# Kernel tuning notes

Measured on AMD Instinct MI355X. Metric: run time of the kernel, lower is better.

Reference implementation:

```python
import jax, jax.numpy as jnp
import numpy as np

N, D, O, H, T, S, R, BN = 4096, 256, 256, 256, 512, 8, 4, 2  # nodes, in, out, hidden, text_len, adj_size, relations used, basis_num


def setup_inputs() -> dict:
    key = jax.random.key(0)
    ks = jax.random.split(key, 16)
    sc = 0.05
    return {
        "entity_embeddings": jax.random.normal(ks[0], (N, D), jnp.float32) * sc,
        "text_encodings": jax.random.normal(ks[1], (1, T, 2 * H), jnp.float32) * sc,
        "adj_to_use": jnp.arange(R, dtype=jnp.int32),
        "adj_masks": jax.random.randint(ks[2], (R, N, N), 0, 2, dtype=jnp.int32),
        "text_guids": jax.random.normal(ks[3], (S, 2 * H), jnp.float32) * sc,
        "graph_guids_1": jax.random.normal(ks[4], (S, D), jnp.float32) * sc,
        "graph_guids_2": jax.random.normal(ks[5], (S, D), jnp.float32) * sc,
        "guid_a": jax.random.normal(ks[6], (S,), jnp.float32),
        "basis_V": jax.random.normal(ks[7], (D, BN, O), jnp.float32) * sc,
        "basis_b": jax.random.normal(ks[8], (S, BN), jnp.float32) * sc,
        "W_1": jax.random.normal(ks[9], (2 * H, D), jnp.float32) * sc,
        "W_2": jax.random.normal(ks[10], (2 * H, D), jnp.float32) * sc,
        "ln_gamma": jnp.ones((O,), jnp.float32),
        "ln_beta": jnp.zeros((O,), jnp.float32),
    }


def reference(entity_embeddings, text_encodings, adj_to_use, adj_masks,
              text_guids, graph_guids_1, graph_guids_2, guid_a,
              basis_V, basis_b, W_1, W_2, ln_gamma, ln_beta):
    te = text_encodings[0]                                  # [T, 2H] (batch of 1)
    tg = text_guids[adj_to_use]                             # [R, 2H]
    # text attention: softmax over T, per relation
    att = jax.nn.softmax(te @ tg.T, axis=0)                 # [T, R]
    context = att.T @ te                                    # [R, 2H]
    c1 = context @ W_1                                      # [R, D]
    c2 = context @ W_2
    ga = jax.nn.sigmoid(guid_a[adj_to_use])[:, None]        # [R, 1]
    g1 = ga * graph_guids_1[adj_to_use] + (1.0 - ga) * c1   # [R, D]
    g2 = ga * graph_guids_2[adj_to_use] + (1.0 - ga) * c2
    s1 = entity_embeddings @ g1.T                           # [N, R]
    s2 = entity_embeddings @ g2.T
    # A[r,i,j] = s1[i,r] + s2[j,r], masked softmax over j
    A = s1.T[:, :, None] + s2.T[:, None, :]                 # [R, N, N]
    A = jnp.where(adj_masks == 1, A, jnp.float32(-1e10))
    A = jax.nn.softmax(A, axis=-1)
    fused = jnp.einsum('rij,jd->rid', A, entity_embeddings) # [R, N, D]
    # torch.cat over relations on last dim -> column index r*D + d
    fused_cat = jnp.transpose(fused, (1, 0, 2)).reshape(N, R * D)
    # torch.matmul([R,BN],[D,BN,O]) -> [D,R,O], then .view(R*D, O) (row index d*R + r)
    bb = basis_b[adj_to_use]                                # [R, BN]
    W = jnp.einsum('rb,dbo->dro', bb, basis_V).reshape(D * R, O)
    out = fused_cat @ W                                     # [N, O]
    mu = jnp.mean(out, axis=-1, keepdims=True)
    var = jnp.var(out, axis=-1, keepdims=True)
    out = (out - mu) / jnp.sqrt(var + 1e-5) * ln_gamma + ln_beta
    return jax.nn.relu(out)
```

## Files before the change

kernel.cpp:

```cpp
#include <hip/hip_runtime.h>
#include <hip/hip_bf16.h>


typedef unsigned short u16;
typedef short bf16x8 __attribute__((ext_vector_type(8)));
typedef float f32x4 __attribute__((ext_vector_type(4)));
typedef int   v4i   __attribute__((ext_vector_type(4)));
typedef unsigned int v2u __attribute__((ext_vector_type(2)));

#define G2_OFF    0
#define E2_OFF    4096
#define WRT_OFF   69632
#define FPT_OFF   593920
#define FUSED_OFF 9506816
#define CAN_OFF   26284032

#define C_ENT 0
#define C_TE  1048576
#define C_TG  1310720
#define C_GG2 1314816
#define C_GA  1316864
#define C_BV  1316872
#define C_BB  1447944
#define C_W2  1447960
#define C_GAM 1579032
#define C_BET 1579288

__device__ __forceinline__ float b2f(u16 u) {
    union { unsigned int i; float f; } v; v.i = ((unsigned int)u) << 16; return v.f;
}
__device__ __forceinline__ u16 f2b(float f) {
    union { float f; unsigned int i; } v; v.f = f;
    return (u16)((v.i + 0x7FFFu + ((v.i >> 16) & 1u)) >> 16);
}

__global__ __launch_bounds__(256) void k_cvt(
    const void* s0, const void* s1, const void* s2, const void* s3,
    const void* s4, const void* s5, const void* s6, const void* s7,
    const void* s8, const void* s9, const unsigned* __restrict__ graw,
    u16* __restrict__ dst)
{
    bool isbf = (graw[0] == 0x3F803F80u);
    const void* srcs[10] = {s0, s1, s2, s3, s4, s5, s6, s7, s8, s9};
    const int ns[10]     = {1048576, 262144, 4096, 2048, 8, 131072, 16, 131072, 256, 256};
    const int offs[10]   = {C_ENT, C_TE, C_TG, C_GG2, C_GA, C_BV, C_BB, C_W2, C_GAM, C_BET};
    const int bstart[11] = {0, 512, 640, 642, 643, 644, 708, 709, 773, 774, 775};
    int b = blockIdx.x, a = 0;
    while (b >= bstart[a + 1]) ++a;
    int rel = b - bstart[a];
    int n = ns[a];
    u16* d = dst + offs[a];
    int base = rel * 2048 + threadIdx.x;
    if (isbf) {
        const u16* s = (const u16*)srcs[a];
        for (int k = 0; k < 8; ++k) { int i = base + k * 256; if (i < n) d[i] = s[i]; }
    } else {
        const float* s = (const float*)srcs[a];
        for (int k = 0; k < 8; ++k) { int i = base + k * 256; if (i < n) d[i] = f2b(s[i]); }
    }
}

__global__ __launch_bounds__(1024) void k_pre(const u16* __restrict__ te,
                                              const int* __restrict__ adj,
                                              const u16* __restrict__ tguids,
                                              const u16* __restrict__ gg2,
                                              const u16* __restrict__ guida,
                                              const u16* __restrict__ W2,
                                              float* __restrict__ g2ws) {
    __shared__ float s_tg[4 * 512];
    __shared__ float s_att[512 * 4];
    __shared__ float s_red[512 * 4];
    __shared__ float s_ctx[4 * 512];
    int tid = threadIdx.x;
    int a[4] = {adj[0], adj[1], adj[2], adj[3]};
    for (int idx = tid; idx < 2048; idx += 1024) {
        int r = idx >> 9, h = idx & 511;
        s_tg[r * 512 + h] = b2f(tguids[a[r] * 512 + h]);
    }
    __syncthreads();
    if (tid < 512) {
        float s[4] = {0.f, 0.f, 0.f, 0.f};
        const u16* row = te + tid * 512;
        for (int h = 0; h < 512; ++h) {
            float tv = b2f(row[h]);
            s[0] += tv * s_tg[h]; s[1] += tv * s_tg[512 + h];
            s[2] += tv * s_tg[1024 + h]; s[3] += tv * s_tg[1536 + h];
        }
        for (int r = 0; r < 4; ++r) { s_att[tid * 4 + r] = s[r]; s_red[tid * 4 + r] = s[r]; }
    }
    __syncthreads();
    for (int st = 256; st > 0; st >>= 1) {
        if (tid < st) for (int r = 0; r < 4; ++r)
            s_red[tid * 4 + r] = fmaxf(s_red[tid * 4 + r], s_red[(tid + st) * 4 + r]);
        __syncthreads();
    }
    float mx[4]; for (int r = 0; r < 4; ++r) mx[r] = s_red[r];
    __syncthreads();
    if (tid < 512) for (int r = 0; r < 4; ++r) {
        float e = __expf(s_att[tid * 4 + r] - mx[r]);
        s_att[tid * 4 + r] = e; s_red[tid * 4 + r] = e;
    }
    __syncthreads();
    for (int st = 256; st > 0; st >>= 1) {
        if (tid < st) for (int r = 0; r < 4; ++r)
            s_red[tid * 4 + r] += s_red[(tid + st) * 4 + r];
        __syncthreads();
    }
    float dn[4]; for (int r = 0; r < 4; ++r) dn[r] = s_red[r];
    __syncthreads();
    if (tid < 512) for (int r = 0; r < 4; ++r) s_att[tid * 4 + r] /= dn[r];
    __syncthreads();
    for (int rep = 0; rep < 2; ++rep) {
        int o = tid + rep * 1024; int r = o >> 9, h = o & 511;
        float acc = 0.f;
        for (int t = 0; t < 512; ++t) acc += s_att[t * 4 + r] * b2f(te[t * 512 + h]);
        s_ctx[r * 512 + h] = acc;
    }
    __syncthreads();
    {
        int r = tid >> 8, d = tid & 255;
        float acc = 0.f;
        for (int h = 0; h < 512; ++h) acc += s_ctx[r * 512 + h] * b2f(W2[h * 256 + d]);
        float gav = 1.f / (1.f + expf(-b2f(guida[a[r]])));
        g2ws[r * 256 + d] = gav * b2f(gg2[a[r] * 256 + d]) + (1.f - gav) * acc;
    }
}

__global__ __launch_bounds__(256) void k_s2_wrt(const u16* __restrict__ entity,
                                                const int* __restrict__ adj,
                                                const u16* __restrict__ basisV,
                                                const u16* __restrict__ basisb,
                                                const float* __restrict__ g2ws,
                                                float* __restrict__ e2ws,
                                                u16* __restrict__ wrt) {
    int b = blockIdx.x, tid = threadIdx.x;
    if (b < 64) {
        int j = b * 64 + (tid >> 2), r = tid & 3;
        const u16* erow = entity + j * 256;
        const float* g2r = g2ws + r * 256;
        float acc = 0.f;
        for (int d = 0; d < 256; ++d) acc += b2f(erow[d]) * g2r[d];
        e2ws[r * 4096 + j] = expf(acc);
    } else {
        int b2 = b - 64; int r = b2 >> 6;
        int c = (b2 & 63) * 4 + (tid >> 6);
        int dq = tid & 63;
        int dbase = dq * 4;
        int a[4] = {adj[0], adj[1], adj[2], adj[3]};
        for (int dd = 0; dd < 4; ++dd) {
            float w = 0.f;
            for (int bi = 0; bi < 2; ++bi)
                w += b2f(basisb[a[dd] * 2 + bi]) * b2f(basisV[((64 * r + dq) * 2 + bi) * 256 + c]);
            wrt[(r * 256 + c) * 256 + dbase + dd] = f2b(w);
        }
    }
}

__global__ __launch_bounds__(256) void k_fplus(const u16* __restrict__ entity,
                                               const u16* __restrict__ wrt,
                                               const float* __restrict__ e2ws,
                                               u16* __restrict__ fpt) {
    int b = blockIdx.x, tid = threadIdx.x;
    if (b < 256) {
        int r = b & 3, ct = (b >> 2) & 3, jt = b >> 4;
        int c0 = ct * 64, j0 = jt * 256;
        __shared__ __align__(16) u16 lw[64 * 264];
        const u16* wr = wrt + (r * 256 + c0) * 256;
        for (int k = 0; k < 8; ++k) {
            int ci = tid + k * 256; int row = ci >> 5, off = (ci & 31) * 8;
            *(v4i*)(&lw[row * 264 + off]) = *(const v4i*)(wr + row * 256 + off);
        }
        __syncthreads();
        int wave = tid >> 6, ln = tid & 15, q = (tid & 63) >> 4;
        f32x4 acc[4][4] = {};
        for (int ks = 0; ks < 8; ++ks) {
            bf16x8 afr[4], bfr[4];
            for (int mt = 0; mt < 4; ++mt)
                afr[mt] = *(const bf16x8*)(&lw[(mt * 16 + ln) * 264 + ks * 32 + q * 8]);
            for (int nt = 0; nt < 4; ++nt) {
                int j = j0 + (wave * 4 + nt) * 16 + ln;
                bfr[nt] = *(const bf16x8*)(entity + j * 256 + ks * 32 + q * 8);
            }
            for (int mt = 0; mt < 4; ++mt)
                for (int nt = 0; nt < 4; ++nt)
                    acc[mt][nt] = __builtin_amdgcn_mfma_f32_16x16x32_bf16(afr[mt], bfr[nt], acc[mt][nt], 0, 0, 0);
        }
        for (int nt = 0; nt < 4; ++nt) {
            int j = j0 + (wave * 4 + nt) * 16 + ln;
            float e2j = e2ws[r * 4096 + j];
            int kt = j >> 5, kk = j & 31;
            u16* dst = fpt + (((size_t)(r * 128 + kt)) * 272 << 5);
            for (int mt = 0; mt < 4; ++mt)
                for (int reg = 0; reg < 4; ++reg) {
                    int c = c0 + mt * 16 + q * 4 + reg;
                    dst[(c << 5) + kk] = f2b(acc[mt][nt][reg] * e2j);
                }
        }
    } else {
        int b2 = b - 256; int r = b2 >> 1, half = b2 & 1;
        const float* e2r = e2ws + r * 4096;
        for (int it = 0; it < 128; ++it) {
            int l = it * 256 + tid;
            int kk = l & 31;
            int c  = 256 + ((l >> 5) & 15);
            int kt = half * 64 + (l >> 9);
            fpt[(((size_t)(r * 128 + kt) * 272 + c) << 5) + kk] =
                (c == 256) ? f2b(e2r[kt * 32 + kk]) : (u16)0;
        }
    }
}

__global__ __launch_bounds__(512) void k_big(const int* __restrict__ masks,
                                             const u16* __restrict__ fpt,
                                             float* __restrict__ fused) {
    __shared__ __align__(16) u16 lm[64 * 40];
    __shared__ __align__(16) u16 lf[272 * 40];
    __shared__ float lden[64];
    int b = blockIdx.x, tid = threadIdx.x;
    int xcd = b & 7; int r = xcd & 3;
    int it = (b >> 3) + ((xcd >> 2) << 5);
    long i0 = (long)it * 64;
    const int* mbase = masks + ((long)r << 24) + i0 * 4096;
    const u16* fbase = fpt + (size_t)r * 128 * 272 * 32;
    int mrow = tid >> 3, mch = tid & 7;
    int wave = tid >> 6, lane = tid & 63, ln = lane & 15, q = lane >> 4;
    int mg = wave >> 2, ng = wave & 3;

    f32x4 acc[2][4] = {};
    f32x4 accD0 = {}, accD1 = {};

    v4i pmA, pf0A, pf1A, pf2A, pmB, pf0B, pf1B, pf2B;
    auto load_into = [&](int kt, v4i& pm_, v4i& p0, v4i& p1, v4i& p2) {
        pm_ = __builtin_nontemporal_load((const v4i*)(mbase + mrow * 4096 + kt * 32 + mch * 4));
        const u16* su = fbase + (size_t)kt * 8704;
        p0 = *(const v4i*)(su + tid * 8);
        p1 = *(const v4i*)(su + (tid + 512) * 8);
        if (tid < 64) p2 = *(const v4i*)(su + (tid + 1024) * 8);
    };
    auto step = [&](int kt, v4i& pm_, v4i& p0, v4i& p1, v4i& p2) {
        __syncthreads();
        {
            unsigned int m0 = (unsigned)pm_.x * 0x3F80u, m1 = (unsigned)pm_.y * 0x3F80u;
            unsigned int m2 = (unsigned)pm_.z * 0x3F80u, m3 = (unsigned)pm_.w * 0x3F80u;
            v2u w; w.x = m0 | (m1 << 16); w.y = m2 | (m3 << 16);
            *(v2u*)(&lm[mrow * 40 + mch * 4]) = w;
        }
        *(v4i*)(&lf[(tid >> 2) * 40 + (tid & 3) * 8]) = p0;
        { int ci = tid + 512; *(v4i*)(&lf[(ci >> 2) * 40 + (ci & 3) * 8]) = p1; }
        if (tid < 64) { int ci = tid + 1024; *(v4i*)(&lf[(ci >> 2) * 40 + (ci & 3) * 8]) = p2; }
        __syncthreads();
        if (kt + 2 < 128) load_into(kt + 2, pm_, p0, p1, p2);
        bf16x8 a0 = *(const bf16x8*)(&lm[(mg * 32 + ln) * 40 + q * 8]);
        bf16x8 a1 = *(const bf16x8*)(&lm[(mg * 32 + 16 + ln) * 40 + q * 8]);
        #pragma unroll
        for (int nt = 0; nt < 4; ++nt) {
            bf16x8 bf = *(const bf16x8*)(&lf[((ng * 4 + nt) * 16 + ln) * 40 + q * 8]);
            acc[0][nt] = __builtin_amdgcn_mfma_f32_16x16x32_bf16(a0, bf, acc[0][nt], 0, 0, 0);
            acc[1][nt] = __builtin_amdgcn_mfma_f32_16x16x32_bf16(a1, bf, acc[1][nt], 0, 0, 0);
        }
        if (ng == 3) {
            bf16x8 bf = *(const bf16x8*)(&lf[(256 + ln) * 40 + q * 8]);
            accD0 = __builtin_amdgcn_mfma_f32_16x16x32_bf16(a0, bf, accD0, 0, 0, 0);
            accD1 = __builtin_amdgcn_mfma_f32_16x16x32_bf16(a1, bf, accD1, 0, 0, 0);
        }
    };

    load_into(0, pmA, pf0A, pf1A, pf2A);
    load_into(1, pmB, pf0B, pf1B, pf2B);
    #pragma unroll 1
    for (int kt = 0; kt < 128; kt += 2) {
        step(kt,     pmA, pf0A, pf1A, pf2A);
        step(kt + 1, pmB, pf0B, pf1B, pf2B);
    }

    if (ng == 3 && ln == 0) {
        #pragma unroll
        for (int reg = 0; reg < 4; ++reg) {
            lden[mg * 32 + q * 4 + reg]      = accD0[reg];
            lden[mg * 32 + 16 + q * 4 + reg] = accD1[reg];
        }
    }
    __syncthreads();
    float* fb = fused + ((long)r * 4096 + i0) * 256;
    #pragma unroll
    for (int mt = 0; mt < 2; ++mt) {
        float rd[4];
        #pragma unroll
        for (int reg = 0; reg < 4; ++reg) rd[reg] = 1.0f / lden[mg * 32 + mt * 16 + q * 4 + reg];
        #pragma unroll
        for (int nt = 0; nt < 4; ++nt) {
            int c = (ng * 4 + nt) * 16 + ln;
            #pragma unroll
            for (int reg = 0; reg < 4; ++reg) {
                int row = mg * 32 + mt * 16 + q * 4 + reg;
                __builtin_nontemporal_store(acc[mt][nt][reg] * rd[reg], fb + row * 256 + c);
            }
        }
    }
}

__global__ __launch_bounds__(256) void k_ln(const float* __restrict__ fused,
                                            const u16* __restrict__ gamma,
                                            const u16* __restrict__ beta,
                                            const unsigned* __restrict__ graw,
                                            void* __restrict__ outraw) {
    __shared__ float red[256];
    int i = blockIdx.x, o = threadIdx.x;
    float x = 0.f;
    for (int r = 0; r < 4; ++r)
        x += __builtin_nontemporal_load(fused + ((long)(r << 12) + i) * 256 + o);
    red[o] = x; __syncthreads();
    for (int st = 128; st > 0; st >>= 1) { if (o < st) red[o] += red[o + st]; __syncthreads(); }
    float mu = red[0] * (1.f / 256.f);
    __syncthreads();
    float v = x - mu;
    red[o] = v * v; __syncthreads();
    for (int st = 128; st > 0; st >>= 1) { if (o < st) red[o] += red[o + st]; __syncthreads(); }
    float var = red[0] * (1.f / 256.f);
    float y = v * rsqrtf(var + 1e-5f) * b2f(gamma[o]) + b2f(beta[o]);
    float res = fmaxf(y, 0.f);
    bool isbf = (graw[0] == 0x3F803F80u);
    if (isbf) ((u16*)outraw)[i * 256 + o] = f2b(res);
    else      ((float*)outraw)[i * 256 + o] = res;
}

extern "C" void kernel_launch(void* const* d_in, const int* in_sizes, int n_in,
                              void* d_out, int out_size, void* d_ws, size_t ws_size,
                              hipStream_t stream) {
    const int* adj   = (const int*)d_in[2];
    const int* masks = (const int*)d_in[3];
    const unsigned* graw = (const unsigned*)d_in[12];
    char* ws = (char*)d_ws;
    float* g2ws = (float*)(ws + G2_OFF);
    float* e2ws = (float*)(ws + E2_OFF);
    u16*   wrt  = (u16*)(ws + WRT_OFF);
    u16*   fpt  = (u16*)(ws + FPT_OFF);
    float* fus  = (float*)(ws + FUSED_OFF);
    u16*   can  = (u16*)(ws + CAN_OFF);

    k_cvt<<<775, 256, 0, stream>>>(d_in[0], d_in[1], d_in[4], d_in[6], d_in[7],
                                   d_in[8], d_in[9], d_in[11], d_in[12], d_in[13],
                                   graw, can);
    const u16* entity = can + C_ENT;
    const u16* te     = can + C_TE;
    const u16* tguids = can + C_TG;
    const u16* gg2    = can + C_GG2;
    const u16* guida  = can + C_GA;
    const u16* basisV = can + C_BV;
    const u16* basisb = can + C_BB;
    const u16* W2     = can + C_W2;
    const u16* gamma  = can + C_GAM;
    const u16* beta   = can + C_BET;

    k_pre<<<1, 1024, 0, stream>>>(te, adj, tguids, gg2, guida, W2, g2ws);
    k_s2_wrt<<<320, 256, 0, stream>>>(entity, adj, basisV, basisb, g2ws, e2ws, wrt);
    k_fplus<<<264, 256, 0, stream>>>(entity, wrt, e2ws, fpt);
    k_big<<<256, 512, 0, stream>>>(masks, fpt, fus);
    k_ln<<<4096, 256, 0, stream>>>(fus, gamma, beta, graw, d_out);
}
```

Before: 551.3 us.

## Split text-attention preprocessing, double-buffer LDS in main GEMM, shuffle-reduce layernorm

The single-block preprocessing kernel is split into three kernels (attention softmax, context, and guided projection), so the context and W2 projections run across several blocks instead of one, and the text rows are read with vector loads. The main masked GEMM now uses two LDS buffers, so the next tile is written while MFMAs consume the current one, needing one barrier per step instead of two. The unpadded layout may add LDS bank conflicts. Layernorm switches to wave shuffles with a one-pass sum and sum of squares, which is slightly less numerically robust.

```diff
diff --git a/kernel.cpp b/kernel.cpp
--- a/kernel.cpp
+++ b/kernel.cpp
@@ -14,6 +14,8 @@
 #define FPT_OFF   593920
 #define FUSED_OFF 9506816
 #define CAN_OFF   26284032
+#define ATT_OFF   29443584
+#define CTX_OFF   29451776
 
 #define C_ENT 0
 #define C_TE  1048576
@@ -32,6 +34,10 @@
 __device__ __forceinline__ u16 f2b(float f) {
     union { float f; unsigned int i; } v; v.f = f;
     return (u16)((v.i + 0x7FFFu + ((v.i >> 16) & 1u)) >> 16);
+}
+__device__ __forceinline__ void bsync() {
+    __builtin_amdgcn_s_waitcnt(0xC07F);
+    __builtin_amdgcn_s_barrier();
 }
 
 __global__ __launch_bounds__(256) void k_cvt(
@@ -60,31 +66,32 @@
     }
 }
 
-__global__ __launch_bounds__(1024) void k_pre(const u16* __restrict__ te,
-                                              const int* __restrict__ adj,
-                                              const u16* __restrict__ tguids,
-                                              const u16* __restrict__ gg2,
-                                              const u16* __restrict__ guida,
-                                              const u16* __restrict__ W2,
-                                              float* __restrict__ g2ws) {
+__global__ __launch_bounds__(512) void k_pre(const u16* __restrict__ te,
+                                             const int* __restrict__ adj,
+                                             const u16* __restrict__ tguids,
+                                             float* __restrict__ att_ws) {
     __shared__ float s_tg[4 * 512];
     __shared__ float s_att[512 * 4];
     __shared__ float s_red[512 * 4];
-    __shared__ float s_ctx[4 * 512];
     int tid = threadIdx.x;
     int a[4] = {adj[0], adj[1], adj[2], adj[3]};
-    for (int idx = tid; idx < 2048; idx += 1024) {
-        int r = idx >> 9, h = idx & 511;
+    for (int k = 0; k < 4; ++k) {
+        int idx = tid + k * 512; int r = idx >> 9, h = idx & 511;
         s_tg[r * 512 + h] = b2f(tguids[a[r] * 512 + h]);
     }
     __syncthreads();
-    if (tid < 512) {
+    {
         float s[4] = {0.f, 0.f, 0.f, 0.f};
         const u16* row = te + tid * 512;
-        for (int h = 0; h < 512; ++h) {
-            float tv = b2f(row[h]);
-            s[0] += tv * s_tg[h]; s[1] += tv * s_tg[512 + h];
-            s[2] += tv * s_tg[1024 + h]; s[3] += tv * s_tg[1536 + h];
+        for (int h8 = 0; h8 < 512; h8 += 8) {
+            v4i pk = *(const v4i*)(row + h8);
+            const u16* pu = (const u16*)&pk;
+            #pragma unroll
+            for (int j = 0; j < 8; ++j) {
+                float tv = b2f(pu[j]);
+                s[0] += tv * s_tg[h8 + j];        s[1] += tv * s_tg[512 + h8 + j];
+                s[2] += tv * s_tg[1024 + h8 + j]; s[3] += tv * s_tg[1536 + h8 + j];
+            }
         }
         for (int r = 0; r < 4; ++r) { s_att[tid * 4 + r] = s[r]; s_red[tid * 4 + r] = s[r]; }
     }
@@ -96,7 +103,7 @@
     }
     float mx[4]; for (int r = 0; r < 4; ++r) mx[r] = s_red[r];
     __syncthreads();
-    if (tid < 512) for (int r = 0; r < 4; ++r) {
+    for (int r = 0; r < 4; ++r) {
         float e = __expf(s_att[tid * 4 + r] - mx[r]);
         s_att[tid * 4 + r] = e; s_red[tid * 4 + r] = e;
     }
@@ -107,23 +114,39 @@
         __syncthreads();
     }
     float dn[4]; for (int r = 0; r < 4; ++r) dn[r] = s_red[r];
-    __syncthreads();
-    if (tid < 512) for (int r = 0; r < 4; ++r) s_att[tid * 4 + r] /= dn[r];
-    __syncthreads();
-    for (int rep = 0; rep < 2; ++rep) {
-        int o = tid + rep * 1024; int r = o >> 9, h = o & 511;
-        float acc = 0.f;
-        for (int t = 0; t < 512; ++t) acc += s_att[t * 4 + r] * b2f(te[t * 512 + h]);
-        s_ctx[r * 512 + h] = acc;
-    }
-    __syncthreads();
-    {
-        int r = tid >> 8, d = tid & 255;
-        float acc = 0.f;
-        for (int h = 0; h < 512; ++h) acc += s_ctx[r * 512 + h] * b2f(W2[h * 256 + d]);
-        float gav = 1.f / (1.f + expf(-b2f(guida[a[r]])));
-        g2ws[r * 256 + d] = gav * b2f(gg2[a[r] * 256 + d]) + (1.f - gav) * acc;
-    }
+    for (int r = 0; r < 4; ++r) att_ws[tid * 4 + r] = s_att[tid * 4 + r] / dn[r];
+}
+
+__global__ __launch_bounds__(256) void k_ctx(const u16* __restrict__ te,
+                                             const float* __restrict__ att,
+                                             float* __restrict__ ctx) {
+    __shared__ float s_att[2048];
+    int tid = threadIdx.x, b = blockIdx.x;
+    for (int k = 0; k < 8; ++k) s_att[tid + k * 256] = att[tid + k * 256];
+    __syncthreads();
+    int r = tid >> 6, h = b * 64 + (tid & 63);
+    float acc = 0.f;
+    #pragma unroll 4
+    for (int t = 0; t < 512; ++t) acc += s_att[t * 4 + r] * b2f(te[t * 512 + h]);
+    ctx[r * 512 + h] = acc;
+}
+
+__global__ __launch_bounds__(256) void k_g2(const float* __restrict__ ctx,
+                                            const int* __restrict__ adj,
+                                            const u16* __restrict__ gg2,
+                                            const u16* __restrict__ guida,
+                                            const u16* __restrict__ W2,
+                                            float* __restrict__ g2ws) {
+    __shared__ float s_c[512];
+    int r = blockIdx.x, d = threadIdx.x;
+    s_c[d] = ctx[r * 512 + d]; s_c[d + 256] = ctx[r * 512 + 256 + d];
+    __syncthreads();
+    float acc = 0.f;
+    #pragma unroll 4
+    for (int h = 0; h < 512; ++h) acc += s_c[h] * b2f(W2[h * 256 + d]);
+    int a = adj[r];
+    float gav = 1.f / (1.f + expf(-b2f(guida[a])));
+    g2ws[r * 256 + d] = gav * b2f(gg2[a * 256 + d]) + (1.f - gav) * acc;
 }
 
 __global__ __launch_bounds__(256) void k_s2_wrt(const u16* __restrict__ entity,
@@ -213,8 +236,8 @@
 __global__ __launch_bounds__(512) void k_big(const int* __restrict__ masks,
                                              const u16* __restrict__ fpt,
                                              float* __restrict__ fused) {
-    __shared__ __align__(16) u16 lm[64 * 40];
-    __shared__ __align__(16) u16 lf[272 * 40];
+    __shared__ __align__(16) u16 lm2[2][64 * 32];
+    __shared__ __align__(16) u16 lf2[2][272 * 32];
     __shared__ float lden[64];
     int b = blockIdx.x, tid = threadIdx.x;
     int xcd = b & 7; int r = xcd & 3;
@@ -229,48 +252,57 @@
     f32x4 acc[2][4] = {};
     f32x4 accD0 = {}, accD1 = {};
 
-    v4i pmA, pf0A, pf1A, pf2A, pmB, pf0B, pf1B, pf2B;
-    auto load_into = [&](int kt, v4i& pm_, v4i& p0, v4i& p1, v4i& p2) {
+    v4i pmA, p0A, p1A, p2A, pmB, p0B, p1B, p2B;
+    auto load_set = [&](int kt, v4i& pm_, v4i& p0, v4i& p1, v4i& p2) {
         pm_ = __builtin_nontemporal_load((const v4i*)(mbase + mrow * 4096 + kt * 32 + mch * 4));
         const u16* su = fbase + (size_t)kt * 8704;
         p0 = *(const v4i*)(su + tid * 8);
-        p1 = *(const v4i*)(su + (tid + 512) * 8);
-        if (tid < 64) p2 = *(const v4i*)(su + (tid + 1024) * 8);
+        p1 = *(const v4i*)(su + 4096 + tid * 8);
+        if (tid < 64) p2 = *(const v4i*)(su + 8192 + tid * 8);
     };
-    auto step = [&](int kt, v4i& pm_, v4i& p0, v4i& p1, v4i& p2) {
-        __syncthreads();
-        {
-            unsigned int m0 = (unsigned)pm_.x * 0x3F80u, m1 = (unsigned)pm_.y * 0x3F80u;
-            unsigned int m2 = (unsigned)pm_.z * 0x3F80u, m3 = (unsigned)pm_.w * 0x3F80u;
-            v2u w; w.x = m0 | (m1 << 16); w.y = m2 | (m3 << 16);
-            *(v2u*)(&lm[mrow * 40 + mch * 4]) = w;
-        }
-        *(v4i*)(&lf[(tid >> 2) * 40 + (tid & 3) * 8]) = p0;
-        { int ci = tid + 512; *(v4i*)(&lf[(ci >> 2) * 40 + (ci & 3) * 8]) = p1; }
-        if (tid < 64) { int ci = tid + 1024; *(v4i*)(&lf[(ci >> 2) * 40 + (ci & 3) * 8]) = p2; }
-        __syncthreads();
-        if (kt + 2 < 128) load_into(kt + 2, pm_, p0, p1, p2);
-        bf16x8 a0 = *(const bf16x8*)(&lm[(mg * 32 + ln) * 40 + q * 8]);
-        bf16x8 a1 = *(const bf16x8*)(&lm[(mg * 32 + 16 + ln) * 40 + q * 8]);
+    auto write_set = [&](int buf, const v4i& pm_, const v4i& p0, const v4i& p1, const v4i& p2) {
+        unsigned m0 = (unsigned)pm_.x * 0x3F80u, m1 = (unsigned)pm_.y * 0x3F80u;
+        unsigned m2 = (unsigned)pm_.z * 0x3F80u, m3 = (unsigned)pm_.w * 0x3F80u;
+        v2u w; w.x = m0 | (m1 << 16); w.y = m2 | (m3 << 16);
+        *(v2u*)(&lm2[buf][mrow * 32 + mch * 4]) = w;
+        *(v4i*)(&lf2[buf][tid * 8]) = p0;
+        *(v4i*)(&lf2[buf][4096 + tid * 8]) = p1;
+        if (tid < 64) *(v4i*)(&lf2[buf][8192 + tid * 8]) = p2;
+    };
+    auto mfma_step = [&](int buf) {
+        const u16* lm = lm2[buf];
+        const u16* lf = lf2[buf];
+        bf16x8 a0 = *(const bf16x8*)(lm + (mg * 32 + ln) * 32 + q * 8);
+        bf16x8 a1 = *(const bf16x8*)(lm + (mg * 32 + 16 + ln) * 32 + q * 8);
         #pragma unroll
         for (int nt = 0; nt < 4; ++nt) {
-            bf16x8 bf = *(const bf16x8*)(&lf[((ng * 4 + nt) * 16 + ln) * 40 + q * 8]);
+            bf16x8 bf = *(const bf16x8*)(lf + ((ng * 4 + nt) * 16 + ln) * 32 + q * 8);
             acc[0][nt] = __builtin_amdgcn_mfma_f32_16x16x32_bf16(a0, bf, acc[0][nt], 0, 0, 0);
             acc[1][nt] = __builtin_amdgcn_mfma_f32_16x16x32_bf16(a1, bf, acc[1][nt], 0, 0, 0);
         }
         if (ng == 3) {
-            bf16x8 bf = *(const bf16x8*)(&lf[(256 + ln) * 40 + q * 8]);
+            bf16x8 bf = *(const bf16x8*)(lf + (256 + ln) * 32 + q * 8);
             accD0 = __builtin_amdgcn_mfma_f32_16x16x32_bf16(a0, bf, accD0, 0, 0, 0);
             accD1 = __builtin_amdgcn_mfma_f32_16x16x32_bf16(a1, bf, accD1, 0, 0, 0);
         }
     };
 
-    load_into(0, pmA, pf0A, pf1A, pf2A);
-    load_into(1, pmB, pf0B, pf1B, pf2B);
+    load_set(0, pmA, p0A, p1A, p2A);
+    load_set(1, pmB, p0B, p1B, p2B);
+    write_set(0, pmA, p0A, p1A, p2A);
+    load_set(2, pmA, p0A, p1A, p2A);
+    bsync();
+
     #pragma unroll 1
     for (int kt = 0; kt < 128; kt += 2) {
-        step(kt,     pmA, pf0A, pf1A, pf2A);
-        step(kt + 1, pmB, pf0B, pf1B, pf2B);
+        write_set(1, pmB, p0B, p1B, p2B);
+        if (kt + 3 < 128) load_set(kt + 3, pmB, p0B, p1B, p2B);
+        mfma_step(0);
+        bsync();
+        if (kt + 2 < 128) write_set(0, pmA, p0A, p1A, p2A);
+        if (kt + 4 < 128) load_set(kt + 4, pmA, p0A, p1A, p2A);
+        mfma_step(1);
+        bsync();
     }
 
     if (ng == 3 && ln == 0) {
@@ -280,7 +312,7 @@
             lden[mg * 32 + 16 + q * 4 + reg] = accD1[reg];
         }
     }
-    __syncthreads();
+    bsync();
     float* fb = fused + ((long)r * 4096 + i0) * 256;
     #pragma unroll
     for (int mt = 0; mt < 2; ++mt) {
@@ -304,20 +336,21 @@
                                             const u16* __restrict__ beta,
                                             const unsigned* __restrict__ graw,
                                             void* __restrict__ outraw) {
-    __shared__ float red[256];
-    int i = blockIdx.x, o = threadIdx.x;
+    __shared__ float wsum[4], wsum2[4];
+    int i = blockIdx.x, o = threadIdx.x, w = o >> 6, l = o & 63;
     float x = 0.f;
     for (int r = 0; r < 4; ++r)
         x += __builtin_nontemporal_load(fused + ((long)(r << 12) + i) * 256 + o);
-    red[o] = x; __syncthreads();
-    for (int st = 128; st > 0; st >>= 1) { if (o < st) red[o] += red[o + st]; __syncthreads(); }
-    float mu = red[0] * (1.f / 256.f);
-    __syncthreads();
-    float v = x - mu;
-    red[o] = v * v; __syncthreads();
-    for (int st = 128; st > 0; st >>= 1) { if (o < st) red[o] += red[o + st]; __syncthreads(); }
-    float var = red[0] * (1.f / 256.f);
-    float y = v * rsqrtf(var + 1e-5f) * b2f(gamma[o]) + b2f(beta[o]);
+    float s = x, s2 = x * x;
+    #pragma unroll
+    for (int d = 1; d < 64; d <<= 1) { s += __shfl_xor(s, d); s2 += __shfl_xor(s2, d); }
+    if (l == 0) { wsum[w] = s; wsum2[w] = s2; }
+    __syncthreads();
+    float tot  = wsum[0] + wsum[1] + wsum[2] + wsum[3];
+    float tot2 = wsum2[0] + wsum2[1] + wsum2[2] + wsum2[3];
+    float mu = tot * (1.f / 256.f);
+    float var = tot2 * (1.f / 256.f) - mu * mu;
+    float y = (x - mu) * rsqrtf(var + 1e-5f) * b2f(gamma[o]) + b2f(beta[o]);
     float res = fmaxf(y, 0.f);
     bool isbf = (graw[0] == 0x3F803F80u);
     if (isbf) ((u16*)outraw)[i * 256 + o] = f2b(res);
@@ -337,6 +370,8 @@
     u16*   fpt  = (u16*)(ws + FPT_OFF);
     float* fus  = (float*)(ws + FUSED_OFF);
     u16*   can  = (u16*)(ws + CAN_OFF);
+    float* attw = (float*)(ws + ATT_OFF);
+    float* ctxw = (float*)(ws + CTX_OFF);
 
     k_cvt<<<775, 256, 0, stream>>>(d_in[0], d_in[1], d_in[4], d_in[6], d_in[7],
                                    d_in[8], d_in[9], d_in[11], d_in[12], d_in[13],
@@ -352,7 +387,9 @@
     const u16* gamma  = can + C_GAM;
     const u16* beta   = can + C_BET;
 
-    k_pre<<<1, 1024, 0, stream>>>(te, adj, tguids, gg2, guida, W2, g2ws);
+    k_pre<<<1, 512, 0, stream>>>(te, adj, tguids, attw);
+    k_ctx<<<8, 256, 0, stream>>>(te, attw, ctxw);
+    k_g2<<<4, 256, 0, stream>>>(ctxw, adj, gg2, guida, W2, g2ws);
     k_s2_wrt<<<320, 256, 0, stream>>>(entity, adj, basisV, basisb, g2ws, e2ws, wrt);
     k_fplus<<<264, 256, 0, stream>>>(entity, wrt, e2ws, fpt);
     k_big<<<256, 512, 0, stream>>>(masks, fpt, fus);
```

After: 560.5 us. About the same (+1.7%).
